# Performance work log

Measured on AMD Instinct MI355X. Metric: run time of the kernel, lower is better.

## Reference

```python
import jax, jax.numpy as jnp
import numpy as np

N = 500_000            # nodes
E = 16_000_000         # used edges (var edges); E_total = 2*E
EPS = 1e-5             # BatchNorm eps
SQRT_C = np.sqrt(2.0).astype(np.float32)  # out_channels=2


def setup_inputs() -> dict:
    key = jax.random.key(0)
    ks = jax.random.split(key, 20)
    w = lambda k, s: (jax.random.normal(k, s, jnp.float32) * 0.5)
    d = {}
    d["x"] = jax.random.normal(ks[0], (N, 2), jnp.float32)
    d["edge_index"] = jax.random.randint(ks[1], (2, 2 * E), 0, N, jnp.int32)
    d["edge_attr"] = jax.random.normal(ks[2], (2 * E, 2), jnp.float32)
    d["mask"] = (jax.random.uniform(ks[3], (N,)) < 0.5).astype(jnp.float32)
    # TransformerConv(2,2,edge_dim=2,heads=1) params
    d["Wq"], d["bq"] = w(ks[4], (2, 2)), w(ks[5], (2,))
    d["Wk"], d["bk"] = w(ks[6], (2, 2)), w(ks[7], (2,))
    d["Wv"], d["bv"] = w(ks[8], (2, 2)), w(ks[9], (2,))
    d["We"] = w(ks[10], (2, 2))               # lin_edge, bias=False
    d["Wskip"], d["bskip"] = w(ks[11], (2, 2)), w(ks[12], (2,))
    # BatchNorm(2) affine params
    d["gamma"], d["beta"] = jnp.ones((2,), jnp.float32), jnp.zeros((2,), jnp.float32)
    # final Linear(2,1)
    d["Wf"], d["bf"] = w(ks[13], (1, 2)), w(ks[14], (1,))
    return d


def _transformer_conv(x, src, dst, ea, Wq, bq, Wk, bk, Wv, bv, We, Wskip, bskip):
    # PyG TransformerConv, heads=1, concat=True, root_weight=True, beta=False
    q = x @ Wq.T + bq                       # [N,2]
    k = x @ Wk.T + bk                       # [N,2]
    v = x @ Wv.T + bv                       # [N,2]
    e = ea @ We.T                           # [E,2]
    k_j = k[src] + e                        # [E,2]
    alpha = jnp.sum(q[dst] * k_j, axis=1) / SQRT_C  # [E]
    # segment softmax over destination nodes
    m = jax.ops.segment_max(alpha, dst, num_segments=N)          # -inf for empty
    m = jnp.where(jnp.isfinite(m), m, 0.0)
    a = jnp.exp(alpha - m[dst])
    s = jax.ops.segment_sum(a, dst, num_segments=N)
    wgt = a / jnp.where(s[dst] > 0, s[dst], 1.0)                 # [E]
    msg = (v[src] + e) * wgt[:, None]                            # [E,2]
    out = jax.ops.segment_sum(msg, dst, num_segments=N)          # [N,2]
    return out + x @ Wskip.T + bskip


def _neighbor_max(x, src, dst, ea_clause):
    # vectorized form of the per-node Python loop (scatter-max)
    s = jnp.sum(x[src] * ea_clause, axis=1)                      # [E]
    seg = jax.ops.segment_max(s, dst, num_segments=N)            # [N]
    deg = jax.ops.segment_sum(jnp.ones_like(s), dst, num_segments=N)
    has = deg > 0
    mx = jnp.where(has, seg, 0.0)
    stacked = jnp.stack([mx, 1.0 - mx], axis=1)                  # [N,2]
    return jnp.where(has[:, None], stacked, x)


def reference(x, edge_index, edge_attr, mask, Wq, bq, Wk, bk, Wv, bv, We,
              Wskip, bskip, gamma, beta, Wf, bf):
    ei = edge_index[:, 1::2]        # var_index = odd columns
    ea = edge_attr[1::2]            # var edge attrs
    ea_clause = edge_attr[0::2]     # clause edge attrs
    src, dst = ei[0], ei[1]
    h = _transformer_conv(x, src, dst, ea, Wq, bq, Wk, bk, Wv, bv, We, Wskip, bskip)
    # BatchNorm1d, training-mode batch statistics (biased var)
    mu = jnp.mean(h, axis=0)
    var = jnp.mean((h - mu) ** 2, axis=0)
    h = (h - mu) / jnp.sqrt(var + EPS) * gamma + beta
    # softmax over node dim (dim=0)
    h = jax.nn.softmax(h, axis=0)
    h = _neighbor_max(h, src, dst, ea_clause)
    # iterations=1 -> extra loop body does not execute
    out = jnp.squeeze(h @ Wf.T + bf)       # [N]
    return out * mask
```

## Files before the change

### kernel.cpp

```cpp
#include <hip/hip_runtime.h>
#include <hip/hip_fp16.h>

#define NNODES 500000
#define NEDGES 16000000
#define NBLK 1024
#define EPB (NEDGES / NBLK)
#define BSH 9
#define BSZ 512
#define NBKT 977
#define BDIM 1024

typedef unsigned long long u64;
typedef unsigned int u32;


__device__ __forceinline__ u32 fmap_ord(float x) {
    u32 u = __float_as_uint(x);
    return (u & 0x80000000u) ? ~u : (u | 0x80000000u);
}
__device__ __forceinline__ float funmap_ord(u32 u) {
    u32 bits = (u & 0x80000000u) ? (u ^ 0x80000000u) : ~u;
    return __uint_as_float(bits);
}

__device__ __forceinline__ void block_reduce_atomic4(float v0, float v1, float v2, float v3,
                                                     float* dst) {
    for (int off = 32; off > 0; off >>= 1) {
        v0 += __shfl_down(v0, off, 64);
        v1 += __shfl_down(v1, off, 64);
        v2 += __shfl_down(v2, off, 64);
        v3 += __shfl_down(v3, off, 64);
    }
    __shared__ float red[4][4];
    int lane = threadIdx.x & 63, wid = threadIdx.x >> 6;
    if (lane == 0) { red[wid][0] = v0; red[wid][1] = v1; red[wid][2] = v2; red[wid][3] = v3; }
    __syncthreads();
    if (threadIdx.x < 4) {
        float t = red[0][threadIdx.x] + red[1][threadIdx.x] + red[2][threadIdx.x] + red[3][threadIdx.x];
        unsafeAtomicAdd(&dst[threadIdx.x], t);
    }
}


__global__ __launch_bounds__(64) void k_zero_accum(float* accum) {
    if (threadIdx.x < 16) accum[threadIdx.x] = 0.f;
}

__global__ __launch_bounds__(256) void k_node_prep(
    const float* __restrict__ x,
    const float* __restrict__ Wq, const float* __restrict__ bq,
    const float* __restrict__ Wk, const float* __restrict__ bk,
    const float* __restrict__ Wv, const float* __restrict__ bv,
    float2* __restrict__ q, float4* __restrict__ kv) {
    int i = blockIdx.x * blockDim.x + threadIdx.x;
    if (i >= NNODES) return;
    float2 xv = ((const float2*)x)[i];
    float q0 = fmaf(Wq[0], xv.x, fmaf(Wq[1], xv.y, bq[0]));
    float q1 = fmaf(Wq[2], xv.x, fmaf(Wq[3], xv.y, bq[1]));
    float k0 = fmaf(Wk[0], xv.x, fmaf(Wk[1], xv.y, bk[0]));
    float k1 = fmaf(Wk[2], xv.x, fmaf(Wk[3], xv.y, bk[1]));
    float v0 = fmaf(Wv[0], xv.x, fmaf(Wv[1], xv.y, bv[0]));
    float v1 = fmaf(Wv[2], xv.x, fmaf(Wv[3], xv.y, bv[1]));
    q[i] = make_float2(q0, q1);
    kv[i] = make_float4(k0, k1, v0, v1);
}

__global__ void k_ln_final(const float* __restrict__ gamma, const float* __restrict__ beta,
                           float* __restrict__ accum) {
    float n = (float)NNODES;
    float mu0 = accum[0] / n, mu1 = accum[1] / n;
    float var0 = accum[2] / n - mu0 * mu0;
    float var1 = accum[3] / n - mu1 * mu1;
    float sc0 = gamma[0] * rsqrtf(var0 + 1e-5f);
    float sc1 = gamma[1] * rsqrtf(var1 + 1e-5f);
    accum[8] = sc0;
    accum[9] = sc1;
    accum[10] = beta[0] - mu0 * sc0;
    accum[11] = beta[1] - mu1 * sc1;
}

__global__ __launch_bounds__(256) void k_softmax(
    const float2* __restrict__ h, float2* __restrict__ pp, float* __restrict__ accum) {
    int i = blockIdx.x * blockDim.x + threadIdx.x;
    float p0 = 0.f, p1 = 0.f;
    if (i < NNODES) {
        float sc0 = accum[8], sc1 = accum[9], sh0 = accum[10], sh1 = accum[11];
        float2 hv = h[i];
        p0 = __expf(fmaf(hv.x, sc0, sh0));
        p1 = __expf(fmaf(hv.y, sc1, sh1));
        pp[i] = make_float2(p0, p1);
    }
    block_reduce_atomic4(p0, p1, 0.f, 0.f, accum + 4);
}

__global__ void k_sm_final(float* __restrict__ accum) {
    accum[12] = 1.f / accum[4];
    accum[13] = 1.f / accum[5];
}


__global__ __launch_bounds__(256) void k_hist(const int2* __restrict__ dst2, u32* __restrict__ M) {
    __shared__ u32 hist[BDIM];
    for (int j = threadIdx.x; j < BDIM; j += 256) hist[j] = 0u;
    __syncthreads();
    int beg = blockIdx.x * EPB, end = beg + EPB;
    #pragma unroll 4
    for (int e = beg + threadIdx.x; e < end; e += 256)
        atomicAdd(&hist[dst2[e].y >> BSH], 1u);
    __syncthreads();
    u32* row = M + (size_t)blockIdx.x * BDIM;
    for (int j = threadIdx.x; j < BDIM; j += 256) row[j] = hist[j];
}

__global__ __launch_bounds__(256) void k_bucket_prefix(u32* __restrict__ M, u32* __restrict__ bucketTotal) {
    __shared__ u32 col[NBLK];
    int b = blockIdx.x;
    for (int j = threadIdx.x; j < NBLK; j += 256) col[j] = M[(size_t)j * BDIM + b];
    __syncthreads();
    if (threadIdx.x == 0) {
        u32 run = 0;
        for (int j = 0; j < NBLK; ++j) { u32 c = col[j]; col[j] = run; run += c; }
        bucketTotal[b] = run;
    }
    __syncthreads();
    for (int j = threadIdx.x; j < NBLK; j += 256) M[(size_t)j * BDIM + b] = col[j];
}

__global__ __launch_bounds__(256) void k_scan_serial(const u32* __restrict__ bucketTotal,
                                                     u32* __restrict__ bucketBase) {
    __shared__ u32 t[BDIM];
    __shared__ u32 o[BDIM + 1];
    for (int j = threadIdx.x; j < BDIM; j += 256) t[j] = bucketTotal[j];
    __syncthreads();
    if (threadIdx.x == 0) {
        u32 run = 0;
        for (int j = 0; j < BDIM; ++j) { o[j] = run; run += t[j]; }
        o[BDIM] = run;
    }
    __syncthreads();
    for (int j = threadIdx.x; j < BDIM + 1; j += 256) bucketBase[j] = o[j];
}


__global__ __launch_bounds__(256) void k_scatter16(
    const int2* __restrict__ src2, const int2* __restrict__ dst2,
    const float4* __restrict__ ea4, const float* __restrict__ We,
    const u32* __restrict__ M, const u32* __restrict__ bucketBase,
    float4* __restrict__ R) {
    __shared__ u32 cur[BDIM];
    const u32* row = M + (size_t)blockIdx.x * BDIM;
    for (int j = threadIdx.x; j < BDIM; j += 256) cur[j] = row[j] + bucketBase[j];
    __syncthreads();
    float we00 = We[0], we01 = We[1], we10 = We[2], we11 = We[3];
    int beg = blockIdx.x * EPB, end = beg + EPB;
    #pragma unroll 4
    for (int e = beg + threadIdx.x; e < end; e += 256) {
        int si = src2[e].y;
        int di = dst2[e].y;
        float4 eav = ea4[e];
        float e0 = fmaf(we00, eav.z, we01 * eav.w);
        float e1 = fmaf(we10, eav.z, we11 * eav.w);
        __half2 hc = __floats2half2_rn(eav.x, eav.y);
        u32 pos = atomicAdd(&cur[di >> BSH], 1u);
        u32 idx = (u32)si | ((u32)(di & (BSZ - 1)) << 19);
        R[pos] = make_float4(__uint_as_float(idx), e0, e1,
                             __uint_as_float(*(u32*)&hc));
    }
}

__global__ __launch_bounds__(256) void k_attn16(
    const float4* __restrict__ R,
    const u32* __restrict__ bucketBase, const u32* __restrict__ bucketTotal,
    const float4* __restrict__ kv, const float2* __restrict__ qp,
    const float* __restrict__ x,
    const float* __restrict__ Wskip, const float* __restrict__ bskip,
    float2* __restrict__ h, float* __restrict__ accum) {
    __shared__ float sA[BSZ], m0A[BSZ], m1A[BSZ];
    __shared__ float2 qT[BSZ];
    int b = blockIdx.x, base = b << BSH;
    for (int j = threadIdx.x; j < BSZ; j += 256) {
        sA[j] = 0.f; m0A[j] = 0.f; m1A[j] = 0.f;
        int i = base + j;
        qT[j] = (i < NNODES) ? qp[i] : make_float2(0.f, 0.f);
    }
    __syncthreads();
    int beg = bucketBase[b], end = beg + bucketTotal[b];
    for (int idx = beg + threadIdx.x; idx < end; idx += 256) {
        float4 r = R[idx];
        u32 rec = __float_as_uint(r.x);
        int si = rec & 0x7FFFFu;
        int li = rec >> 19;
        float4 kvv = kv[si];
        float2 qv = qT[li];
        float alpha = fmaf(qv.x, kvv.x + r.y, qv.y * (kvv.y + r.z)) * 0.70710678118654752f;
        float a = __expf(alpha);
        atomicAdd(&sA[li], a);
        atomicAdd(&m0A[li], a * (kvv.z + r.y));
        atomicAdd(&m1A[li], a * (kvv.w + r.z));
    }
    __syncthreads();
    float r0 = 0.f, r1 = 0.f, r2 = 0.f, r3 = 0.f;
    float w00 = Wskip[0], w01 = Wskip[1], w10 = Wskip[2], w11 = Wskip[3];
    float c0 = bskip[0], c1 = bskip[1];
    for (int j = threadIdx.x; j < BSZ; j += 256) {
        int i = base + j;
        if (i < NNODES) {
            float2 xv = ((const float2*)x)[i];
            float s = sA[j];
            float inv = s > 0.f ? 1.f / s : 0.f;
            float h0 = fmaf(m0A[j], inv, fmaf(w00, xv.x, fmaf(w01, xv.y, c0)));
            float h1 = fmaf(m1A[j], inv, fmaf(w10, xv.x, fmaf(w11, xv.y, c1)));
            h[i] = make_float2(h0, h1);
            r0 += h0; r1 += h1; r2 += h0 * h0; r3 += h1 * h1;
        }
    }
    block_reduce_atomic4(r0, r1, r2, r3, accum);
}

__global__ __launch_bounds__(256) void k_nmax16(
    const float4* __restrict__ R,
    const u32* __restrict__ bucketBase, const u32* __restrict__ bucketTotal,
    const float2* __restrict__ pp, const float* __restrict__ accum,
    const float* __restrict__ Wf, const float* __restrict__ bf,
    const float* __restrict__ mask, float* __restrict__ out) {
    __shared__ u32 mxA[BSZ];
    __shared__ float maskT[BSZ];
    int b = blockIdx.x, base = b << BSH;
    for (int j = threadIdx.x; j < BSZ; j += 256) {
        mxA[j] = 0u;
        int i = base + j;
        maskT[j] = (i < NNODES) ? mask[i] : 0.f;
    }
    __syncthreads();
    float inv0 = accum[12], inv1 = accum[13];
    int beg = bucketBase[b], end = beg + bucketTotal[b];
    for (int idx = beg + threadIdx.x; idx < end; idx += 256) {
        float4 r = R[idx];
        u32 rec = __float_as_uint(r.x);
        int li = rec >> 19;
        if (maskT[li] == 0.f) continue;
        int si = rec & 0x7FFFFu;
        u32 hcbits = __float_as_uint(r.w);
        __half2 hc = *(__half2*)&hcbits;
        float2 cf = __half22float2(hc);
        float2 pv = pp[si];
        float sE = fmaf(pv.x * inv0, cf.x, pv.y * inv1 * cf.y);
        atomicMax(&mxA[li], fmap_ord(sE));
    }
    __syncthreads();
    float wf0 = Wf[0], wf1 = Wf[1], bb = bf[0];
    for (int j = threadIdx.x; j < BSZ; j += 256) {
        int i = base + j;
        if (i >= NNODES) continue;
        u32 m = mxA[j];
        float h0, h1;
        if (m != 0u) { float v = funmap_ord(m); h0 = v; h1 = 1.f - v; }
        else { float2 pv = pp[i]; h0 = pv.x * inv0; h1 = pv.y * inv1; }
        out[i] = fmaf(wf0, h0, fmaf(wf1, h1, bb)) * maskT[j];
    }
}


__global__ __launch_bounds__(256) void k_init_f(float* s, float* msg, u32* mxb, float* accum) {
    int i = blockIdx.x * blockDim.x + threadIdx.x;
    if (i < NNODES) { s[i] = 0.f; mxb[i] = 0u; }
    if (i < 2 * NNODES) msg[i] = 0.f;
    if (i < 16) accum[i] = 0.f;
}

__global__ __launch_bounds__(256) void k_edge_attn_f(
    const int* __restrict__ ei, const float* __restrict__ ea,
    const float* __restrict__ We,
    const float2* __restrict__ q, const float4* __restrict__ kv,
    float* __restrict__ s, float* __restrict__ msg) {
    int e = blockIdx.x * blockDim.x + threadIdx.x;
    if (e >= NEDGES) return;
    float we00 = We[0], we01 = We[1], we10 = We[2], we11 = We[3];
    int si = ((const int2*)ei)[e].y;
    int di = ((const int2*)(ei + 2 * NEDGES))[e].y;
    float2 eav = ((const float2*)ea)[2 * e + 1];
    float4 kvv = kv[si];
    float2 qv = q[di];
    float e0 = fmaf(we00, eav.x, we01 * eav.y);
    float e1 = fmaf(we10, eav.x, we11 * eav.y);
    float alpha = fmaf(qv.x, kvv.x + e0, qv.y * (kvv.y + e1)) * 0.70710678118654752f;
    float a = __expf(alpha);
    unsafeAtomicAdd(&s[di], a);
    unsafeAtomicAdd(&msg[2 * di], a * (kvv.z + e0));
    unsafeAtomicAdd(&msg[2 * di + 1], a * (kvv.w + e1));
}

__global__ __launch_bounds__(256) void k_node_h_f(
    const float* __restrict__ x,
    const float* __restrict__ Wskip, const float* __restrict__ bskip,
    const float* __restrict__ s, float* __restrict__ msg, float* __restrict__ accum) {
    int i = blockIdx.x * blockDim.x + threadIdx.x;
    float h0 = 0.f, h1 = 0.f;
    if (i < NNODES) {
        float2 xv = ((const float2*)x)[i];
        float sk0 = fmaf(Wskip[0], xv.x, fmaf(Wskip[1], xv.y, bskip[0]));
        float sk1 = fmaf(Wskip[2], xv.x, fmaf(Wskip[3], xv.y, bskip[1]));
        float sv = s[i];
        float inv = sv > 0.f ? 1.f / sv : 0.f;
        h0 = fmaf(msg[2 * i], inv, sk0);
        h1 = fmaf(msg[2 * i + 1], inv, sk1);
        msg[2 * i] = h0;
        msg[2 * i + 1] = h1;
    }
    block_reduce_atomic4(h0, h1, h0 * h0, h1 * h1, accum);
}

__global__ __launch_bounds__(256) void k_edge_nmax_f(
    const int* __restrict__ ei, const float* __restrict__ ea,
    const float2* __restrict__ pp, const float* __restrict__ accum,
    u32* __restrict__ mxb) {
    int e = blockIdx.x * blockDim.x + threadIdx.x;
    if (e >= NEDGES) return;
    float inv0 = accum[12], inv1 = accum[13];
    int si = ((const int2*)ei)[e].y;
    int di = ((const int2*)(ei + 2 * NEDGES))[e].y;
    float2 c = ((const float2*)ea)[2 * e];
    float2 pv = pp[si];
    float sE = fmaf(pv.x * inv0, c.x, pv.y * inv1 * c.y);
    atomicMax(&mxb[di], fmap_ord(sE));
}

__global__ __launch_bounds__(256) void k_final_f(
    const u32* __restrict__ mxb, const float2* __restrict__ pp,
    const float* __restrict__ accum,
    const float* __restrict__ Wf, const float* __restrict__ bf,
    const float* __restrict__ mask, float* __restrict__ out) {
    int i = blockIdx.x * blockDim.x + threadIdx.x;
    if (i >= NNODES) return;
    u32 m = mxb[i];
    float h0, h1;
    if (m != 0u) {
        float v = funmap_ord(m);
        h0 = v;
        h1 = 1.f - v;
    } else {
        float2 pv = pp[i];
        h0 = pv.x * accum[12];
        h1 = pv.y * accum[13];
    }
    out[i] = fmaf(Wf[0], h0, fmaf(Wf[1], h1, bf[0])) * mask[i];
}


extern "C" void kernel_launch(void* const* d_in, const int* in_sizes, int n_in,
                              void* d_out, int out_size, void* d_ws, size_t ws_size,
                              hipStream_t stream) {
    const float* x     = (const float*)d_in[0];
    const int*   ei    = (const int*)d_in[1];
    const float* ea    = (const float*)d_in[2];
    const float* mask  = (const float*)d_in[3];
    const float* Wq    = (const float*)d_in[4];
    const float* bq    = (const float*)d_in[5];
    const float* Wk    = (const float*)d_in[6];
    const float* bk    = (const float*)d_in[7];
    const float* Wv    = (const float*)d_in[8];
    const float* bv    = (const float*)d_in[9];
    const float* We    = (const float*)d_in[10];
    const float* Wskip = (const float*)d_in[11];
    const float* bskip = (const float*)d_in[12];
    const float* gamma = (const float*)d_in[13];
    const float* beta  = (const float*)d_in[14];
    const float* Wf    = (const float*)d_in[15];
    const float* bf    = (const float*)d_in[16];
    float* out = (float*)d_out;

    const size_t N = NNODES;
    const size_t E = NEDGES;
    const int B = 256;
    const int gridN = (NNODES + B - 1) / B;

    const int2*   src2 = (const int2*)ei;
    const int2*   dst2 = (const int2*)(ei + 2 * NEDGES);
    const float4* ea4  = (const float4*)ea;

    size_t need16 = 16 * N
                  + 16 * E
                  + 8 * N
                  + 8 * N
                  + 8 * N
                  + 4 * (size_t)NBLK * BDIM
                  + 4 * BDIM
                  + 4 * (BDIM + 16)
                  + 64;

    if (ws_size >= need16) {
        char* base = (char*)d_ws;
        float4* kv = (float4*)base;                 base += 16 * N;
        float4* R  = (float4*)base;                 base += 16 * E;
        float2* q  = (float2*)base;                 base += 8 * N;
        float2* h  = (float2*)base;                 base += 8 * N;
        float2* p  = (float2*)base;                 base += 8 * N;
        u32*    M  = (u32*)base;                    base += 4 * (size_t)NBLK * BDIM;
        u32*    bT = (u32*)base;                    base += 4 * BDIM;
        u32*    bB = (u32*)base;                    base += 4 * (BDIM + 16);
        float*  accum = (float*)base;

        k_zero_accum<<<1, 64, 0, stream>>>(accum);
        k_node_prep<<<gridN, B, 0, stream>>>(x, Wq, bq, Wk, bk, Wv, bv, q, kv);
        k_hist<<<NBLK, B, 0, stream>>>(dst2, M);
        k_bucket_prefix<<<BDIM, B, 0, stream>>>(M, bT);
        k_scan_serial<<<1, B, 0, stream>>>(bT, bB);
        k_scatter16<<<NBLK, B, 0, stream>>>(src2, dst2, ea4, We, M, bB, R);
        k_attn16<<<NBKT, B, 0, stream>>>(R, bB, bT, kv, q, x, Wskip, bskip, h, accum);
        k_ln_final<<<1, 1, 0, stream>>>(gamma, beta, accum);
        k_softmax<<<gridN, B, 0, stream>>>(h, p, accum);
        k_sm_final<<<1, 1, 0, stream>>>(accum);
        k_nmax16<<<NBKT, B, 0, stream>>>(R, bB, bT, p, accum, Wf, bf, mask, out);
    } else {
        float*  q   = (float*)d_ws;
        float*  kvf = q + 2 * N;
        float*  s   = kvf + 4 * N;
        float*  msg = s + N;
        u32*    mxb = (u32*)(msg + 2 * N);
        float*  accum = (float*)(mxb + N);
        int grid2N = (int)((2 * N + B - 1) / B);
        int gridE  = (NEDGES + B - 1) / B;

        k_init_f<<<grid2N, B, 0, stream>>>(s, msg, mxb, accum);
        k_node_prep<<<gridN, B, 0, stream>>>(x, Wq, bq, Wk, bk, Wv, bv, (float2*)q, (float4*)kvf);
        k_edge_attn_f<<<gridE, B, 0, stream>>>(ei, ea, We, (const float2*)q, (const float4*)kvf, s, msg);
        k_node_h_f<<<gridN, B, 0, stream>>>(x, Wskip, bskip, s, msg, accum);
        k_ln_final<<<1, 1, 0, stream>>>(gamma, beta, accum);
        k_softmax<<<gridN, B, 0, stream>>>((const float2*)msg, (float2*)q, accum);
        k_sm_final<<<1, 1, 0, stream>>>(accum);
        k_edge_nmax_f<<<gridE, B, 0, stream>>>(ei, ea, (const float2*)q, accum, mxb);
        k_final_f<<<gridN, B, 0, stream>>>(mxb, (const float2*)q, accum, Wf, bf, mask, out);
    }
}
```

Before: 788.8 us.

## Stage bucket scatter through shared memory to coalesce global writes

Rewrites the edge scatter kernel so each block processes 2048-edge chunks. It builds a local histogram, prefix-scans it, and sorts the records by bucket in LDS before writing them to global memory. This way consecutive threads write contiguous runs within each bucket, replacing the old fully random 16-byte scattered stores. The trade-off is about 45KB of shared memory per block, which lowers occupancy, plus several extra barriers and scans per chunk.

```diff
diff --git a/kernel.cpp b/kernel.cpp
--- a/kernel.cpp
+++ b/kernel.cpp
@@ -9,9 +9,12 @@
 #define BSZ 512
 #define NBKT 977
 #define BDIM 1024
+#define CHUNK 2048
+#define KPC (CHUNK / 256)
 
 typedef unsigned long long u64;
 typedef unsigned int u32;
+typedef unsigned short u16;
 
 
 __device__ __forceinline__ u32 fmap_ord(float x) {
@@ -142,29 +145,90 @@
 }
 
 
-__global__ __launch_bounds__(256) void k_scatter16(
+__global__ __launch_bounds__(256) void k_scatter_stg(
     const int2* __restrict__ src2, const int2* __restrict__ dst2,
     const float4* __restrict__ ea4, const float* __restrict__ We,
     const u32* __restrict__ M, const u32* __restrict__ bucketBase,
     float4* __restrict__ R) {
-    __shared__ u32 cur[BDIM];
+    __shared__ u32 hist[BDIM];
+    __shared__ u32 lbase[BDIM];
+    __shared__ u32 gcur[BDIM];
+    __shared__ u32 wsum[4];
+    __shared__ float4 buf[CHUNK];
+    __shared__ u16 bkt[CHUNK];
+
     const u32* row = M + (size_t)blockIdx.x * BDIM;
-    for (int j = threadIdx.x; j < BDIM; j += 256) cur[j] = row[j] + bucketBase[j];
-    __syncthreads();
+    for (int j = threadIdx.x; j < BDIM; j += 256) gcur[j] = row[j] + bucketBase[j];
     float we00 = We[0], we01 = We[1], we10 = We[2], we11 = We[3];
-    int beg = blockIdx.x * EPB, end = beg + EPB;
-    #pragma unroll 4
-    for (int e = beg + threadIdx.x; e < end; e += 256) {
-        int si = src2[e].y;
-        int di = dst2[e].y;
-        float4 eav = ea4[e];
-        float e0 = fmaf(we00, eav.z, we01 * eav.w);
-        float e1 = fmaf(we10, eav.z, we11 * eav.w);
-        __half2 hc = __floats2half2_rn(eav.x, eav.y);
-        u32 pos = atomicAdd(&cur[di >> BSH], 1u);
-        u32 idx = (u32)si | ((u32)(di & (BSZ - 1)) << 19);
-        R[pos] = make_float4(__uint_as_float(idx), e0, e1,
-                             __uint_as_float(*(u32*)&hc));
+    int beg = blockIdx.x * EPB;
+    int lane = threadIdx.x & 63, wid = threadIdx.x >> 6;
+
+    for (int c0 = 0; c0 < EPB; c0 += CHUNK) {
+        int cn = min(CHUNK, EPB - c0);
+        for (int j = threadIdx.x; j < BDIM; j += 256) hist[j] = 0u;
+        __syncthreads();
+
+        float4 recs[KPC]; u32 bks[KPC]; u32 rnk[KPC]; bool val[KPC];
+        #pragma unroll
+        for (int k = 0; k < KPC; ++k) {
+            int tt = k * 256 + threadIdx.x;
+            val[k] = tt < cn;
+            if (val[k]) {
+                int e = beg + c0 + tt;
+                int si = src2[e].y;
+                int di = dst2[e].y;
+                float4 eav = ea4[e];
+                float e0 = fmaf(we00, eav.z, we01 * eav.w);
+                float e1 = fmaf(we10, eav.z, we11 * eav.w);
+                __half2 hc = __floats2half2_rn(eav.x, eav.y);
+                u32 b = (u32)di >> BSH;
+                u32 idx = (u32)si | ((u32)(di & (BSZ - 1)) << 19);
+                recs[k] = make_float4(__uint_as_float(idx), e0, e1,
+                                      __uint_as_float(*(u32*)&hc));
+                bks[k] = b;
+                rnk[k] = atomicAdd(&hist[b], 1u);
+            }
+        }
+        __syncthreads();
+
+        int t4 = threadIdx.x * 4;
+        u32 s0 = hist[t4], s1 = hist[t4 + 1], s2 = hist[t4 + 2], s3 = hist[t4 + 3];
+        u32 tsum = s0 + s1 + s2 + s3;
+        u32 inc = tsum;
+        #pragma unroll
+        for (int d = 1; d < 64; d <<= 1) {
+            u32 v = __shfl_up(inc, d, 64);
+            if (lane >= d) inc += v;
+        }
+        if (lane == 63) wsum[wid] = inc;
+        __syncthreads();
+        u32 woff = 0;
+        for (int w = 0; w < wid; ++w) woff += wsum[w];
+        u32 tbase = woff + inc - tsum;
+        lbase[t4] = tbase;
+        lbase[t4 + 1] = tbase + s0;
+        lbase[t4 + 2] = tbase + s0 + s1;
+        lbase[t4 + 3] = tbase + s0 + s1 + s2;
+        __syncthreads();
+
+        #pragma unroll
+        for (int k = 0; k < KPC; ++k) {
+            if (val[k]) {
+                u32 p = lbase[bks[k]] + rnk[k];
+                buf[p] = recs[k];
+                bkt[p] = (u16)bks[k];
+            }
+        }
+        __syncthreads();
+
+        for (int j = threadIdx.x; j < cn; j += 256) {
+            u32 b = bkt[j];
+            R[(size_t)gcur[b] + (u32)j - lbase[b]] = buf[j];
+        }
+        __syncthreads();
+
+        for (int j = threadIdx.x; j < BDIM; j += 256) gcur[j] += hist[j];
+        __syncthreads();
     }
 }
 
@@ -405,7 +469,7 @@
         k_hist<<<NBLK, B, 0, stream>>>(dst2, M);
         k_bucket_prefix<<<BDIM, B, 0, stream>>>(M, bT);
         k_scan_serial<<<1, B, 0, stream>>>(bT, bB);
-        k_scatter16<<<NBLK, B, 0, stream>>>(src2, dst2, ea4, We, M, bB, R);
+        k_scatter_stg<<<NBLK, B, 0, stream>>>(src2, dst2, ea4, We, M, bB, R);
         k_attn16<<<NBKT, B, 0, stream>>>(R, bB, bT, kv, q, x, Wskip, bskip, h, accum);
         k_ln_final<<<1, 1, 0, stream>>>(gamma, beta, accum);
         k_softmax<<<gridN, B, 0, stream>>>(h, p, accum);
```

New measurement: 776.6 us. About the same (-1.5%).
